# Optimization experiments

Hardware: AMD Instinct MI355X
Metric: run time of the kernel (lower is better)

Reference implementation:

```python
import jax, jax.numpy as jnp
import numpy as np

DIM = 2048
NUM_HEADS = 16
HEAD_DIM = DIM // NUM_HEADS
SCALE = 1.0 / float(np.sqrt(HEAD_DIM))


def setup_inputs() -> dict:
    key = jax.random.key(0)
    ks = jax.random.split(key, 7)
    B, L = 2, 2048
    x = jax.random.normal(ks[0], (B, L, DIM), dtype=jnp.float32)
    s = 1.0 / np.sqrt(DIM)
    # nn.Linear stores weight as [out, in]; y = x @ W.T + b
    Wq = jax.random.uniform(ks[1], (DIM, DIM), jnp.float32, -s, s)
    bq = jax.random.uniform(ks[2], (DIM,), jnp.float32, -s, s)
    Wk = jax.random.uniform(ks[3], (DIM, DIM), jnp.float32, -s, s)
    bk = jax.random.uniform(ks[4], (DIM,), jnp.float32, -s, s)
    Wv = jax.random.uniform(ks[5], (DIM, DIM), jnp.float32, -s, s)
    bv = jax.random.uniform(ks[6], (DIM,), jnp.float32, -s, s)
    return {"x": x, "Wq": Wq, "bq": bq, "Wk": Wk, "bk": bk, "Wv": Wv, "bv": bv}


def _attn(x, Wq, bq, Wk, bk, Wv, bv):
    B, L, D = x.shape
    H, Hd = NUM_HEADS, HEAD_DIM
    # projections: x @ W.T + b, then split heads -> [B, H, L, Hd]
    q = (x @ Wq.T + bq).reshape(B, L, H, Hd).transpose(0, 2, 1, 3)
    k = (x @ Wk.T + bk).reshape(B, L, H, Hd).transpose(0, 2, 1, 3)
    v = (x @ Wv.T + bv).reshape(B, L, H, Hd).transpose(0, 2, 1, 3)
    scores = jnp.einsum("bhqd,bhkd->bhqk", q, k) * SCALE  # [B,H,L,L]
    attn = jax.nn.softmax(scores, axis=-1)
    out = jnp.einsum("bhqk,bhkd->bhqd", attn, v)
    return out.transpose(0, 2, 1, 3).reshape(B, L, D)


def reference(x, Wq, bq, Wk, bk, Wv, bv):
    return _attn(x, Wq, bq, Wk, bk, Wv, bv)
```

## Files before the change

kernel.cpp:

```cpp
#include <hip/hip_runtime.h>
#include <stdint.h>

typedef unsigned short u16;
typedef __attribute__((ext_vector_type(8))) short short8;
typedef __attribute__((ext_vector_type(16))) float f32x16;

#define ATTN_SCALE 0.08838834764831845f

__device__ __forceinline__ u16 f2bf(float f) {
  union { float f; uint32_t u; } a; a.f = f;
  return (u16)((a.u + 0x7fffu + ((a.u >> 16) & 1u)) >> 16);
}

__device__ __forceinline__ void async16(const u16* g, u16* lds) {
  __builtin_amdgcn_global_load_lds(
      (const __attribute__((address_space(1))) void*)g,
      (__attribute__((address_space(3))) void*)lds, 16, 0, 0);
}

__global__ void cvt_kernel(const float* __restrict__ src, u16* __restrict__ dst, int n8) {
  int i = blockIdx.x * 256 + threadIdx.x;
  if (i >= n8) return;
  const float4* s4 = (const float4*)src;
  float4 a = s4[2 * i], c = s4[2 * i + 1];
  union { u16 h[8]; uint4 v; } o;
  o.h[0] = f2bf(a.x); o.h[1] = f2bf(a.y); o.h[2] = f2bf(a.z); o.h[3] = f2bf(a.w);
  o.h[4] = f2bf(c.x); o.h[5] = f2bf(c.y); o.h[6] = f2bf(c.z); o.h[7] = f2bf(c.w);
  ((uint4*)dst)[i] = o.v;
}

__global__ void cvtw_kernel(const float* __restrict__ w0, const float* __restrict__ w1,
                            const float* __restrict__ w2, u16* __restrict__ dst) {
  int z = blockIdx.y;
  const float* src = (z == 0) ? w0 : (z == 1) ? w1 : w2;
  int i = blockIdx.x * 256 + threadIdx.x;
  const float4* s4 = (const float4*)src;
  float4 a = s4[2 * i], c = s4[2 * i + 1];
  union { u16 h[8]; uint4 v; } o;
  o.h[0] = f2bf(a.x); o.h[1] = f2bf(a.y); o.h[2] = f2bf(a.z); o.h[3] = f2bf(a.w);
  o.h[4] = f2bf(c.x); o.h[5] = f2bf(c.y); o.h[6] = f2bf(c.z); o.h[7] = f2bf(c.w);
  ((uint4*)(dst + (size_t)z * 4194304))[i] = o.v;
}

__global__ __launch_bounds__(256, 4) void qkv_gemm(
    const u16* __restrict__ xb, const u16* __restrict__ Wb,
    const float* __restrict__ bq, const float* __restrict__ bk, const float* __restrict__ bv,
    u16* __restrict__ qkv) {
  __shared__ __align__(16) u16 As[2][128 * 32];
  __shared__ __align__(16) u16 Bs[2][128 * 32];
  const int z = blockIdx.z;
  const int n0 = blockIdx.x * 128, m0 = blockIdx.y * 128;
  const u16* Bw = Wb + (size_t)z * (2048u * 2048u);
  const float* bias = (z == 0) ? bq : (z == 1) ? bk : bv;
  u16* dst = qkv + (size_t)z * 8388608u;
  const int t = threadIdx.x, wave = t >> 6, lane = t & 63;
  const int wm = wave >> 1, wn = wave & 1, l31 = lane & 31, h = lane >> 5;

  int soff[2], goff[2];
#pragma unroll
  for (int p = 0; p < 2; ++p) {
    const int s = p * 256 + wave * 64 + lane;
    const int R = s >> 4, j = s & 15, u = j ^ (R & 15);
    const int m = R * 4 + (u >> 2), c = u & 3;
    soff[p] = s * 8;
    goff[p] = m * 2048 + c * 8;
  }
  int fr16[2][2], fR15[2][2];
  const int q4 = (l31 & 3) * 4;
#pragma unroll
  for (int i = 0; i < 2; ++i) {
    const int mA = wm * 64 + i * 32 + l31, mB = wn * 64 + i * 32 + l31;
    fr16[0][i] = (mA >> 2) * 16; fR15[0][i] = (mA >> 2) & 15;
    fr16[1][i] = (mB >> 2) * 16; fR15[1][i] = (mB >> 2) & 15;
  }

  f32x16 acc[2][2];
#pragma unroll
  for (int i = 0; i < 2; ++i)
#pragma unroll
    for (int j = 0; j < 2; ++j)
#pragma unroll
      for (int r = 0; r < 16; ++r) acc[i][j][r] = 0.f;

  const u16* Abase = xb + (size_t)m0 * 2048;
  const u16* Bbase = Bw + (size_t)n0 * 2048;

#pragma unroll 1
  for (int n = 0; n < 64; ++n) {
    if (n == 0) {
#pragma unroll
      for (int p = 0; p < 2; ++p) {
        async16(Abase + goff[p], &As[0][soff[p]]);
        async16(Bbase + goff[p], &Bs[0][soff[p]]);
      }
    }
    __syncthreads();
    const int cur = n & 1;
    if (n + 1 < 64) {
      const int k1 = (n + 1) * 32;
#pragma unroll
      for (int p = 0; p < 2; ++p) {
        async16(Abase + goff[p] + k1, &As[cur ^ 1][soff[p]]);
        async16(Bbase + goff[p] + k1, &Bs[cur ^ 1][soff[p]]);
      }
    }
#pragma unroll
    for (int ks = 0; ks < 2; ++ks) {
      const int c = ks * 2 + h;
      short8 af[2], bf[2];
#pragma unroll
      for (int i = 0; i < 2; ++i) {
        af[i] = *(const short8*)&As[cur][(fr16[0][i] + ((q4 + c) ^ fR15[0][i])) * 8];
        bf[i] = *(const short8*)&Bs[cur][(fr16[1][i] + ((q4 + c) ^ fR15[1][i])) * 8];
      }
#pragma unroll
      for (int i = 0; i < 2; ++i)
#pragma unroll
        for (int j = 0; j < 2; ++j)
          acc[i][j] = __builtin_amdgcn_mfma_f32_32x32x16_bf16(af[i], bf[j], acc[i][j], 0, 0, 0);
    }
  }

#pragma unroll
  for (int j = 0; j < 2; ++j) {
    const int col = n0 + wn * 64 + j * 32 + l31;
    const float bb_ = bias[col];
    const int hh = col >> 7, hd = col & 127;
#pragma unroll
    for (int i = 0; i < 2; ++i) {
#pragma unroll
      for (int g = 0; g < 4; ++g) {
        const int lbase = m0 + wm * 64 + i * 32 + 8 * g + 4 * h;
        const int bb = lbase >> 11, l0 = lbase & 2047;
        if (z == 2) {
          union { u16 q[4]; uint2 d; } pk;
#pragma unroll
          for (int rr = 0; rr < 4; ++rr) pk.q[rr] = f2bf(acc[i][j][4 * g + rr] + bb_);
          *(uint2*)&dst[((size_t)(bb * 16 + hh) * 128 + hd) * 2048 + l0] = pk.d;
        } else {
#pragma unroll
          for (int rr = 0; rr < 4; ++rr)
            dst[((size_t)(bb * 16 + hh) * 2048 + (l0 + rr)) * 128 + hd] =
                f2bf(acc[i][j][4 * g + rr] + bb_);
        }
      }
    }
  }
}

__global__ __launch_bounds__(256, 3) void attn_kernel(
    const u16* __restrict__ Qg,
    const u16* __restrict__ Kg,
    const u16* __restrict__ Vtg,
    float* __restrict__ out) {
  __shared__ __align__(16) u16 Ks[64 * 128];
  __shared__ __align__(16) u16 Vs[128 * 64];
  const int bh = blockIdx.y, q0 = blockIdx.x * 128;
  const int t = threadIdx.x, wave = t >> 6, lane = t & 63;
  const int l31 = lane & 31, h = lane >> 5;
  const u16* Qp = Qg + (size_t)bh * 262144;
  const u16* Kp = Kg + (size_t)bh * 262144;
  const u16* Vp = Vtg + (size_t)bh * 262144;
  const int b = bh >> 4, hd = bh & 15;
  const int qrow = q0 + wave * 32 + l31;

  short8 qf[8];
#pragma unroll
  for (int s = 0; s < 8; ++s)
    qf[s] = *(const short8*)&Qp[(size_t)qrow * 128 + s * 16 + h * 8];

  int kOff[4], kSlot[4], vOff[4], vSlot[4];
#pragma unroll
  for (int p = 0; p < 4; ++p) {
    const int s = p * 256 + wave * 64 + lane;
    const int rk = s >> 4, gk = (s & 15) ^ (rk & 15);
    kSlot[p] = s * 8; kOff[p] = rk * 128 + gk * 8;
    const int rv = s >> 3, gv = (s & 7) ^ (rv & 7);
    vSlot[p] = s * 8; vOff[p] = rv * 2048 + gv * 8;
  }

  f32x16 oac[4];
#pragma unroll
  for (int dt = 0; dt < 4; ++dt)
#pragma unroll
    for (int r = 0; r < 16; ++r) oac[dt][r] = 0.f;
  float den = 0.f;

#pragma unroll 1
  for (int kt = 0; kt < 32; ++kt) {
    const int k0 = kt * 64;
    __syncthreads();
#pragma unroll
    for (int p = 0; p < 4; ++p) async16(Kp + (size_t)k0 * 128 + kOff[p], &Ks[kSlot[p]]);
#pragma unroll
    for (int p = 0; p < 4; ++p) async16(Vp + (size_t)k0 + vOff[p], &Vs[vSlot[p]]);
    __syncthreads();

#pragma unroll
    for (int T = 0; T < 2; ++T) {
      const int krow = T * 32 + l31;
      f32x16 sc;
#pragma unroll
      for (int r = 0; r < 16; ++r) sc[r] = 0.f;
#pragma unroll
      for (int s = 0; s < 8; ++s) {
        const short8 kf = *(const short8*)&Ks[(krow * 16 + ((2 * s + h) ^ (krow & 15))) * 8];
        sc = __builtin_amdgcn_mfma_f32_32x32x16_bf16(kf, qf[s], sc, 0, 0, 0);
      }
      uint32_t pp[8];
#pragma unroll
      for (int i = 0; i < 8; ++i) {
        const float e0 = __expf(fminf(sc[2 * i] * ATTN_SCALE, 80.f));
        const float e1 = __expf(fminf(sc[2 * i + 1] * ATTN_SCALE, 80.f));
        den += e0 + e1;
        union { float f; uint32_t u; } u0, u1; u0.f = e0; u1.f = e1;
        pp[i] = ((u1.u + 0x8000u) & 0xffff0000u) | ((u0.u + 0x8000u) >> 16);
      }
      uint32_t x[8];
#pragma unroll
      for (int i = 0; i < 8; ++i) x[i] = __shfl_xor(pp[i], 32, 64);
#pragma unroll
      for (int ks = 0; ks < 2; ++ks) {
        const int o0 = ks * 4;
        union { uint32_t u[4]; short8 s8; } bfp;
        bfp.u[0] = h ? x[o0 + 2] : pp[o0 + 0];
        bfp.u[1] = h ? x[o0 + 3] : pp[o0 + 1];
        bfp.u[2] = h ? pp[o0 + 2] : x[o0 + 0];
        bfp.u[3] = h ? pp[o0 + 3] : x[o0 + 1];
        const int gk = T * 4 + ks * 2 + h;
#pragma unroll
        for (int dt = 0; dt < 4; ++dt) {
          const int vrow = dt * 32 + l31;
          const short8 vf = *(const short8*)&Vs[(vrow * 8 + (gk ^ (vrow & 7))) * 8];
          oac[dt] = __builtin_amdgcn_mfma_f32_32x32x16_bf16(vf, bfp.s8, oac[dt], 0, 0, 0);
        }
      }
    }
  }

  den += __shfl_xor(den, 32, 64);
  const float inv = 1.f / den;
#pragma unroll
  for (int dt = 0; dt < 4; ++dt) {
#pragma unroll
    for (int g4 = 0; g4 < 4; ++g4) {
      float4 o;
      o.x = oac[dt][4 * g4 + 0] * inv;
      o.y = oac[dt][4 * g4 + 1] * inv;
      o.z = oac[dt][4 * g4 + 2] * inv;
      o.w = oac[dt][4 * g4 + 3] * inv;
      const int d = dt * 32 + g4 * 8 + h * 4;
      *(float4*)&out[((size_t)(b * 2048 + qrow)) * 2048 + hd * 128 + d] = o;
    }
  }
}

extern "C" void kernel_launch(void* const* d_in, const int* in_sizes, int n_in,
                              void* d_out, int out_size, void* d_ws, size_t ws_size,
                              hipStream_t stream) {
  const float* x  = (const float*)d_in[0];
  const float* Wq = (const float*)d_in[1];
  const float* bq = (const float*)d_in[2];
  const float* Wk = (const float*)d_in[3];
  const float* bk = (const float*)d_in[4];
  const float* Wv = (const float*)d_in[5];
  const float* bv = (const float*)d_in[6];
  float* out = (float*)d_out;
  if (ws_size < 92274688u) return;

  u16* xb  = (u16*)d_ws;
  u16* Wb  = xb + 8388608;
  u16* qkv = Wb + 12582912;

  cvt_kernel<<<4096, 256, 0, stream>>>(x, xb, 1048576);
  cvtw_kernel<<<dim3(2048, 3), 256, 0, stream>>>(Wq, Wk, Wv, Wb);
  qkv_gemm<<<dim3(16, 32, 3), 256, 0, stream>>>(xb, Wb, bq, bk, bv, qkv);
  attn_kernel<<<dim3(16, 32), 256, 0, stream>>>(qkv, qkv + 8388608, qkv + 16777216, out);
}
```

Before: 351.4 us.

## Double query tile per wave and double-buffer K/V loads in attention

Each wave now processes two 32-row query subtiles, 256 queries per block, so every K and V fragment read from LDS feeds twice as many MFMAs. K/V tiles are double-buffered in LDS: the next tile's async global-to-LDS loads are issued right after the barrier, cutting one barrier per iteration and overlapping loads with compute. The grid halves to 256 blocks, launch bounds drop to one block per CU, and register pressure rises. That leaves only four waves per CU to hide latency.

Measured after the change: 384.7 us. +9.5%, slower.

```diff
diff --git a/kernel.cpp b/kernel.cpp
--- a/kernel.cpp
+++ b/kernel.cpp
@@ -148,26 +148,29 @@
   }
 }
 
-__global__ __launch_bounds__(256, 3) void attn_kernel(
+__global__ __launch_bounds__(256, 1) void attn_kernel(
     const u16* __restrict__ Qg,
     const u16* __restrict__ Kg,
     const u16* __restrict__ Vtg,
     float* __restrict__ out) {
-  __shared__ __align__(16) u16 Ks[64 * 128];
-  __shared__ __align__(16) u16 Vs[128 * 64];
-  const int bh = blockIdx.y, q0 = blockIdx.x * 128;
+  __shared__ __align__(16) u16 Ks[2][64 * 128];
+  __shared__ __align__(16) u16 Vs[2][128 * 64];
+  const int bh = blockIdx.y, q0 = blockIdx.x * 256;
   const int t = threadIdx.x, wave = t >> 6, lane = t & 63;
   const int l31 = lane & 31, h = lane >> 5;
   const u16* Qp = Qg + (size_t)bh * 262144;
   const u16* Kp = Kg + (size_t)bh * 262144;
   const u16* Vp = Vtg + (size_t)bh * 262144;
   const int b = bh >> 4, hd = bh & 15;
-  const int qrow = q0 + wave * 32 + l31;
-
-  short8 qf[8];
-#pragma unroll
-  for (int s = 0; s < 8; ++s)
-    qf[s] = *(const short8*)&Qp[(size_t)qrow * 128 + s * 16 + h * 8];
+
+  short8 qf[2][8];
+#pragma unroll
+  for (int qs = 0; qs < 2; ++qs) {
+    const int qrow = q0 + wave * 64 + qs * 32 + l31;
+#pragma unroll
+    for (int s = 0; s < 8; ++s)
+      qf[qs][s] = *(const short8*)&Qp[(size_t)qrow * 128 + s * 16 + h * 8];
+  }
 
   int kOff[4], kSlot[4], vOff[4], vSlot[4];
 #pragma unroll
@@ -179,78 +182,103 @@
     vSlot[p] = s * 8; vOff[p] = rv * 2048 + gv * 8;
   }
 
-  f32x16 oac[4];
-#pragma unroll
-  for (int dt = 0; dt < 4; ++dt)
-#pragma unroll
-    for (int r = 0; r < 16; ++r) oac[dt][r] = 0.f;
-  float den = 0.f;
+  f32x16 oac[2][4];
+#pragma unroll
+  for (int qs = 0; qs < 2; ++qs)
+#pragma unroll
+    for (int dt = 0; dt < 4; ++dt)
+#pragma unroll
+      for (int r = 0; r < 16; ++r) oac[qs][dt][r] = 0.f;
+  float den[2] = {0.f, 0.f};
 
 #pragma unroll 1
-  for (int kt = 0; kt < 32; ++kt) {
-    const int k0 = kt * 64;
+  for (int n = 0; n < 32; ++n) {
+    if (n == 0) {
+#pragma unroll
+      for (int p = 0; p < 4; ++p) {
+        async16(Kp + kOff[p], &Ks[0][kSlot[p]]);
+        async16(Vp + vOff[p], &Vs[0][vSlot[p]]);
+      }
+    }
     __syncthreads();
-#pragma unroll
-    for (int p = 0; p < 4; ++p) async16(Kp + (size_t)k0 * 128 + kOff[p], &Ks[kSlot[p]]);
-#pragma unroll
-    for (int p = 0; p < 4; ++p) async16(Vp + (size_t)k0 + vOff[p], &Vs[vSlot[p]]);
-    __syncthreads();
+    const int cur = n & 1;
+    if (n + 1 < 32) {
+      const int k1 = (n + 1) * 64;
+#pragma unroll
+      for (int p = 0; p < 4; ++p) {
+        async16(Kp + (size_t)k1 * 128 + kOff[p], &Ks[cur ^ 1][kSlot[p]]);
+        async16(Vp + (size_t)k1 + vOff[p], &Vs[cur ^ 1][vSlot[p]]);
+      }
+    }
 
 #pragma unroll
     for (int T = 0; T < 2; ++T) {
       const int krow = T * 32 + l31;
-      f32x16 sc;
-#pragma unroll
-      for (int r = 0; r < 16; ++r) sc[r] = 0.f;
+      f32x16 sc[2];
+#pragma unroll
+      for (int qs = 0; qs < 2; ++qs)
+#pragma unroll
+        for (int r = 0; r < 16; ++r) sc[qs][r] = 0.f;
 #pragma unroll
       for (int s = 0; s < 8; ++s) {
-        const short8 kf = *(const short8*)&Ks[(krow * 16 + ((2 * s + h) ^ (krow & 15))) * 8];
-        sc = __builtin_amdgcn_mfma_f32_32x32x16_bf16(kf, qf[s], sc, 0, 0, 0);
-      }
-      uint32_t pp[8];
-#pragma unroll
-      for (int i = 0; i < 8; ++i) {
-        const float e0 = __expf(fminf(sc[2 * i] * ATTN_SCALE, 80.f));
-        const float e1 = __expf(fminf(sc[2 * i + 1] * ATTN_SCALE, 80.f));
-        den += e0 + e1;
-        union { float f; uint32_t u; } u0, u1; u0.f = e0; u1.f = e1;
-        pp[i] = ((u1.u + 0x8000u) & 0xffff0000u) | ((u0.u + 0x8000u) >> 16);
-      }
-      uint32_t x[8];
-#pragma unroll
-      for (int i = 0; i < 8; ++i) x[i] = __shfl_xor(pp[i], 32, 64);
+        const short8 kf = *(const short8*)&Ks[cur][(krow * 16 + ((2 * s + h) ^ (krow & 15))) * 8];
+        sc[0] = __builtin_amdgcn_mfma_f32_32x32x16_bf16(kf, qf[0][s], sc[0], 0, 0, 0);
+        sc[1] = __builtin_amdgcn_mfma_f32_32x32x16_bf16(kf, qf[1][s], sc[1], 0, 0, 0);
+      }
+      uint32_t pp[2][8], x[2][8];
+#pragma unroll
+      for (int qs = 0; qs < 2; ++qs) {
+#pragma unroll
+        for (int i = 0; i < 8; ++i) {
+          const float e0 = __expf(fminf(sc[qs][2 * i] * ATTN_SCALE, 80.f));
+          const float e1 = __expf(fminf(sc[qs][2 * i + 1] * ATTN_SCALE, 80.f));
+          den[qs] += e0 + e1;
+          union { float f; uint32_t u; } u0, u1; u0.f = e0; u1.f = e1;
+          pp[qs][i] = ((u1.u + 0x8000u) & 0xffff0000u) | ((u0.u + 0x8000u) >> 16);
+        }
+#pragma unroll
+        for (int i = 0; i < 8; ++i) x[qs][i] = __shfl_xor(pp[qs][i], 32, 64);
+      }
 #pragma unroll
       for (int ks = 0; ks < 2; ++ks) {
         const int o0 = ks * 4;
-        union { uint32_t u[4]; short8 s8; } bfp;
-        bfp.u[0] = h ? x[o0 + 2] : pp[o0 + 0];
-        bfp.u[1] = h ? x[o0 + 3] : pp[o0 + 1];
-        bfp.u[2] = h ? pp[o0 + 2] : x[o0 + 0];
-        bfp.u[3] = h ? pp[o0 + 3] : x[o0 + 1];
+        union { uint32_t u[4]; short8 s8; } bfp[2];
+#pragma unroll
+        for (int qs = 0; qs < 2; ++qs) {
+          bfp[qs].u[0] = h ? x[qs][o0 + 2] : pp[qs][o0 + 0];
+          bfp[qs].u[1] = h ? x[qs][o0 + 3] : pp[qs][o0 + 1];
+          bfp[qs].u[2] = h ? pp[qs][o0 + 2] : x[qs][o0 + 0];
+          bfp[qs].u[3] = h ? pp[qs][o0 + 3] : x[qs][o0 + 1];
+        }
         const int gk = T * 4 + ks * 2 + h;
 #pragma unroll
         for (int dt = 0; dt < 4; ++dt) {
           const int vrow = dt * 32 + l31;
-          const short8 vf = *(const short8*)&Vs[(vrow * 8 + (gk ^ (vrow & 7))) * 8];
-          oac[dt] = __builtin_amdgcn_mfma_f32_32x32x16_bf16(vf, bfp.s8, oac[dt], 0, 0, 0);
+          const short8 vf = *(const short8*)&Vs[cur][(vrow * 8 + (gk ^ (vrow & 7))) * 8];
+          oac[0][dt] = __builtin_amdgcn_mfma_f32_32x32x16_bf16(vf, bfp[0].s8, oac[0][dt], 0, 0, 0);
+          oac[1][dt] = __builtin_amdgcn_mfma_f32_32x32x16_bf16(vf, bfp[1].s8, oac[1][dt], 0, 0, 0);
         }
       }
     }
   }
 
-  den += __shfl_xor(den, 32, 64);
-  const float inv = 1.f / den;
-#pragma unroll
-  for (int dt = 0; dt < 4; ++dt) {
-#pragma unroll
-    for (int g4 = 0; g4 < 4; ++g4) {
-      float4 o;
-      o.x = oac[dt][4 * g4 + 0] * inv;
-      o.y = oac[dt][4 * g4 + 1] * inv;
-      o.z = oac[dt][4 * g4 + 2] * inv;
-      o.w = oac[dt][4 * g4 + 3] * inv;
-      const int d = dt * 32 + g4 * 8 + h * 4;
-      *(float4*)&out[((size_t)(b * 2048 + qrow)) * 2048 + hd * 128 + d] = o;
+#pragma unroll
+  for (int qs = 0; qs < 2; ++qs) {
+    float d2 = den[qs] + __shfl_xor(den[qs], 32, 64);
+    const float inv = 1.f / d2;
+    const int qrow = q0 + wave * 64 + qs * 32 + l31;
+#pragma unroll
+    for (int dt = 0; dt < 4; ++dt) {
+#pragma unroll
+      for (int g4 = 0; g4 < 4; ++g4) {
+        float4 o;
+        o.x = oac[qs][dt][4 * g4 + 0] * inv;
+        o.y = oac[qs][dt][4 * g4 + 1] * inv;
+        o.z = oac[qs][dt][4 * g4 + 2] * inv;
+        o.w = oac[qs][dt][4 * g4 + 3] * inv;
+        const int d = dt * 32 + g4 * 8 + h * 4;
+        *(float4*)&out[((size_t)(b * 2048 + qrow)) * 2048 + hd * 128 + d] = o;
+      }
     }
   }
 }
@@ -275,5 +303,5 @@
   cvt_kernel<<<4096, 256, 0, stream>>>(x, xb, 1048576);
   cvtw_kernel<<<dim3(2048, 3), 256, 0, stream>>>(Wq, Wk, Wv, Wb);
   qkv_gemm<<<dim3(16, 32, 3), 256, 0, stream>>>(xb, Wb, bq, bk, bv, qkv);
-  attn_kernel<<<dim3(16, 32), 256, 0, stream>>>(qkv, qkv + 8388608, qkv + 16777216, out);
-}
+  attn_kernel<<<dim3(8, 32), 256, 0, stream>>>(qkv, qkv + 8388608, qkv + 16777216, out);
+}
```
